# Kernel optimization log

Measured on AMD Instinct MI355X. Metric: run time of the kernel, lower is better.

The kernel has to match this reference:

```python
import jax, jax.numpy as jnp
import numpy as np

DIM = 384
HEADS = 6
NEG = -1e9  # masked-score fill; equivalent to gathering only kept K/V rows


def setup_inputs() -> dict:
    key = jax.random.key(0)
    ks = jax.random.split(key, 9)
    B, N, C = 1, 4098, DIM
    x = jax.random.normal(ks[0], (B, N, C), dtype=jnp.float32)
    pos = jax.random.normal(ks[1], (B, N + 1, C), dtype=jnp.float32)
    # float mask in [0,1); >=0.5 means 'foreground / keep as key', <0.5 pooled into back token
    mask = jax.random.uniform(ks[2], (B, 1, N - 2), dtype=jnp.float32)
    mask_block = jnp.ones((N + 1,), dtype=jnp.float32)  # positions 0, N-1, N always kept
    Wq = jax.random.normal(ks[3], (C, C), dtype=jnp.float32) * 0.02
    Wk = jax.random.normal(ks[4], (C, C), dtype=jnp.float32) * 0.02
    Wv = jax.random.normal(ks[5], (C, C), dtype=jnp.float32) * 0.02
    Wp = jax.random.normal(ks[6], (C, C), dtype=jnp.float32) * 0.02
    bp = jnp.zeros((C,), dtype=jnp.float32)
    return {"x": x, "pos": pos, "mask": mask, "mask_block": mask_block,
            "Wq": Wq, "Wk": Wk, "Wv": Wv, "Wp": Wp, "bp": bp}


def reference(x, pos, mask, mask_block, Wq, Wk, Wv, Wp, bp):
    B, N, C = x.shape
    H = HEADS
    D = C // H
    scale = D ** -0.5
    eps = 1e-10

    # back token: average of background (mask < 0.5) interior tokens
    reverse = jnp.where(mask < 0.5, 1.0, 0.0)                      # (B,1,N-2)
    pooled = jnp.einsum('bon,bnc->boc', reverse, x[:, 1:N - 1])    # (B,1,C)
    back_tokens = pooled / (reverse.sum(axis=2, keepdims=True) + eps)

    kv_x = jnp.concatenate([x, back_tokens], axis=1)               # (B,N+1,C)
    q_x = x + pos[:, :N]
    k_x = kv_x + pos

    q = (q_x @ Wq.T).reshape(B, N, H, D).transpose(0, 2, 1, 3)       # (B,H,N,D)
    k = (k_x @ Wk.T).reshape(B, N + 1, H, D).transpose(0, 2, 1, 3)   # (B,H,N+1,D)
    v = (kv_x @ Wv.T).reshape(B, N + 1, H, D).transpose(0, 2, 1, 3)  # (B,H,N+1,D)

    # key-selection mask: original gathers rows with mask_block >= 0.5;
    # masked softmax over all N+1 keys is mathematically identical.
    mb = mask_block.at[1:N - 1].set(mask[0, 0])
    keep = mb >= 0.5                                               # (N+1,)

    scores = jnp.einsum('bhqd,bhkd->bhqk', q, k) * scale
    scores = jnp.where(keep[None, None, None, :], scores, NEG)
    attn = jax.nn.softmax(scores, axis=-1)
    out = jnp.einsum('bhqk,bhkd->bhqd', attn, v)
    out = out.transpose(0, 2, 1, 3).reshape(B, N, C)
    return out @ Wp.T + bp
```

## Files before the change

### kernel.cpp

```cpp
#include <hip/hip_runtime.h>
#include <math.h>

#define N_TOK 4098
#define NK_TOK 4099
#define C_DIM 384
#define NKPAD 4160
#define NSLICE 5

typedef short  bh8 __attribute__((ext_vector_type(8)));
typedef float  f32x4 __attribute__((ext_vector_type(4)));
typedef unsigned short ushort;
typedef ushort u4 __attribute__((ext_vector_type(4)));
typedef ushort u8 __attribute__((ext_vector_type(8)));

static __device__ __forceinline__ ushort f2bf(float f) {
  unsigned int u = __float_as_uint(f);
  u = (u + 0x7FFF + ((u >> 16) & 1)) >> 16;
  return (ushort)u;
}
static __device__ __forceinline__ float bf2f(ushort s) {
  return __uint_as_float(((unsigned int)s) << 16);
}

#define QSCALE 0.18033688011112042f

__global__ __launch_bounds__(256) void prep_kernel(
    const float* __restrict__ x, const float* __restrict__ pos,
    const float* __restrict__ Wq, const float* __restrict__ Wk,
    const float* __restrict__ Wv, const float* __restrict__ Wp,
    const float* __restrict__ mask, const float* __restrict__ mask_block,
    ushort* __restrict__ Ak, ushort* __restrict__ Av,
    ushort* __restrict__ Wb, int* __restrict__ nk, int* __restrict__ inv,
    float* __restrict__ pooled_part, float* __restrict__ cnt_part) {
  const int b = blockIdx.x, t = threadIdx.x;
  if (b < 260) {
    const int r0 = b * 16;
#pragma unroll
    for (int i = 0; i < 6; ++i) {
      const int idx = i * 1024 + t * 4;
      const int row = r0 + idx / C_DIM, col = idx % C_DIM;
      if (row >= NK_TOK - 1) continue;
      const float4 pv = *(const float4*)&pos[(size_t)row * C_DIM + col];
      const float4 xv = *(const float4*)&x[(size_t)row * C_DIM + col];
      u4 k4 = {f2bf(xv.x + pv.x), f2bf(xv.y + pv.y),
               f2bf(xv.z + pv.z), f2bf(xv.w + pv.w)};
      *(u4*)&Ak[(size_t)row * C_DIM + col] = k4;
      u4 v4 = {f2bf(xv.x), f2bf(xv.y), f2bf(xv.z), f2bf(xv.w)};
      *(u4*)&Av[(size_t)row * C_DIM + col] = v4;
    }
  } else if (b < 292) {
    const int wi = b - 260;
    const float* src = (wi < 8) ? Wq : (wi < 16) ? Wk : (wi < 24) ? Wv : Wp;
    const float sc = (wi < 8) ? QSCALE : 1.f;
    const int base = (wi >> 3) * 147456 + (wi & 7) * 18432;
#pragma unroll 2
    for (int i = 0; i < 18; ++i) {
      const int g = base + i * 1024 + t * 4;
      const float4 v = *(const float4*)&src[(wi & 7) * 18432 + i * 1024 + t * 4];
      u4 o = {f2bf(v.x * sc), f2bf(v.y * sc), f2bf(v.z * sc), f2bf(v.w * sc)};
      *(u4*)&Wb[g] = o;
    }
  } else if (b == 292) {
    __shared__ int scnt[256];
    const int j0 = t * 17;
    unsigned int bits = 0;
    int c = 0;
#pragma unroll 1
    for (int u = 0; u < 17; ++u) {
      const int j = j0 + u;
      bool keep = false;
      if (j < NK_TOK)
        keep = (j >= 1 && j <= N_TOK - 2) ? (mask[j - 1] >= 0.5f)
                                          : (mask_block[j] >= 0.5f);
      if (keep) { bits |= 1u << u; ++c; }
    }
    scnt[t] = c;
    __syncthreads();
    for (int d = 1; d < 256; d <<= 1) {
      const int v = scnt[t];
      const int add = (t >= d) ? scnt[t - d] : 0;
      __syncthreads();
      scnt[t] = v + add;
      __syncthreads();
    }
    int base = scnt[t] - c;
    if (t == 255) *nk = scnt[255];
#pragma unroll 1
    for (int u = 0; u < 17; ++u) {
      const int j = j0 + u;
      if (j < NK_TOK) inv[j] = ((bits >> u) & 1) ? base++ : -1;
    }
  } else {
    const int pb = b - 293;
    const int r0 = pb * 64;
    float acc0 = 0.f, acc1 = 0.f;
    int lc = 0;
    for (int r = r0; r < r0 + 64; ++r) {
      if (mask[r] < 0.5f) {
        acc0 += x[(size_t)(r + 1) * C_DIM + t];
        if (t < 128) acc1 += x[(size_t)(r + 1) * C_DIM + 256 + t];
        ++lc;
      }
    }
    pooled_part[pb * C_DIM + t] = acc0;
    if (t < 128) pooled_part[pb * C_DIM + 256 + t] = acc1;
    if (t == 0) cnt_part[pb] = (float)lc;
  }
}

static __device__ __forceinline__ void gemm_core(
    const ushort* __restrict__ A, const ushort* __restrict__ B,
    ushort (* __restrict__ As)[72], ushort (* __restrict__ Bs)[72],
    int t, int w, int quad, int l15, f32x4 acc[4]) {
  const int g = t & 7;
  u8 ra[2], rb[2];
#pragma unroll
  for (int it = 0; it < 2; ++it) {
    const int r = it * 32 + (t >> 3);
    ra[it] = *(const u8*)&A[r * C_DIM + g * 8];
    rb[it] = *(const u8*)&B[r * C_DIM + g * 8];
  }
#pragma unroll 1
  for (int kt = 0; kt < 6; ++kt) {
    __syncthreads();
#pragma unroll
    for (int it = 0; it < 2; ++it) {
      const int r = it * 32 + (t >> 3);
      *(u8*)&As[r][g * 8] = ra[it];
      *(u8*)&Bs[r][g * 8] = rb[it];
    }
    __syncthreads();
    if (kt < 5) {
      const int k0 = (kt + 1) * 64;
#pragma unroll
      for (int it = 0; it < 2; ++it) {
        const int r = it * 32 + (t >> 3);
        ra[it] = *(const u8*)&A[r * C_DIM + k0 + g * 8];
        rb[it] = *(const u8*)&B[r * C_DIM + k0 + g * 8];
      }
    }
    const bh8 b0 = *(const bh8*)&Bs[w * 16 + l15][quad * 8];
    const bh8 b1 = *(const bh8*)&Bs[w * 16 + l15][32 + quad * 8];
#pragma unroll
    for (int mb = 0; mb < 4; ++mb) {
      const bh8 a0 = *(const bh8*)&As[mb * 16 + l15][quad * 8];
      const bh8 a1 = *(const bh8*)&As[mb * 16 + l15][32 + quad * 8];
      acc[mb] = __builtin_amdgcn_mfma_f32_16x16x32_bf16(a0, b0, acc[mb], 0, 0, 0);
      acc[mb] = __builtin_amdgcn_mfma_f32_16x16x32_bf16(a1, b1, acc[mb], 0, 0, 0);
    }
  }
}

__global__ __launch_bounds__(256) void gemm3_kernel(
    ushort* __restrict__ Ak, ushort* __restrict__ Av,
    const ushort* __restrict__ Wb, const int* __restrict__ inv,
    const float* __restrict__ pooled_part, const float* __restrict__ cnt_part,
    const float* __restrict__ pos,
    ushort* __restrict__ Qh, ushort* __restrict__ Kc, ushort* __restrict__ Vt) {
  __shared__ ushort As[64][72], Bs[64][72];
  const int t = threadIdx.x, w = t >> 6, lane = t & 63;
  const int quad = lane >> 4, l15 = lane & 15;
  const int m0 = blockIdx.x * 64;
  const int which = blockIdx.y / 6, h = blockIdx.y % 6;

  if (blockIdx.x == 64 && which >= 1) {
    float cs = 0.f;
#pragma unroll
    for (int p = 0; p < 64; ++p) cs += cnt_part[p];
    const float ic = 1.f / (cs + 1e-10f);
    for (int c = t; c < C_DIM; c += 256) {
      float s = 0.f;
      for (int p = 0; p < 64; ++p) s += pooled_part[p * C_DIM + c];
      const float back = s * ic;
      const size_t off = (size_t)(NK_TOK - 1) * C_DIM + c;
      if (which == 1) Ak[off] = f2bf(back + pos[off]);
      else            Av[off] = f2bf(back);
    }
    __syncthreads();
  }

  const ushort* A = (which == 2 ? Av : Ak) + (size_t)m0 * C_DIM;
  const ushort* B = Wb + (size_t)which * 147456 + (size_t)h * 64 * C_DIM;
  f32x4 acc[4];
#pragma unroll
  for (int i = 0; i < 4; ++i) acc[i] = (f32x4){0.f, 0.f, 0.f, 0.f};
  gemm_core(A, B, As, Bs, t, w, quad, l15, acc);
  const int n = w * 16 + l15;
  if (which == 0) {
#pragma unroll
    for (int mb = 0; mb < 4; ++mb)
#pragma unroll
      for (int r = 0; r < 4; ++r) {
        const int m = m0 + mb * 16 + quad * 4 + r;
        if (m < N_TOK) Qh[((size_t)h * N_TOK + m) * 64 + n] = f2bf(acc[mb][r]);
      }
  } else if (which == 1) {
#pragma unroll
    for (int mb = 0; mb < 4; ++mb)
#pragma unroll
      for (int r = 0; r < 4; ++r) {
        const int m = m0 + mb * 16 + quad * 4 + r;
        if (m < NK_TOK) {
          const int slot = inv[m];
          if (slot >= 0) Kc[((size_t)h * NKPAD + slot) * 64 + n] = f2bf(acc[mb][r]);
        }
      }
  } else {
#pragma unroll
    for (int mb = 0; mb < 4; ++mb)
#pragma unroll
      for (int r = 0; r < 4; ++r) {
        const int m = m0 + mb * 16 + quad * 4 + r;
        if (m < NK_TOK) {
          const int slot = inv[m];
          if (slot >= 0) Vt[((size_t)h * 64 + n) * NKPAD + slot] = f2bf(acc[mb][r]);
        }
      }
  }
}

__global__ __launch_bounds__(256) void gemm_out_kernel(
    const ushort* __restrict__ Am, const ushort* __restrict__ Wpb,
    const float* __restrict__ bp, float* __restrict__ out) {
  __shared__ ushort As[64][72], Bs[64][72];
  const int t = threadIdx.x, w = t >> 6, lane = t & 63;
  const int quad = lane >> 4, l15 = lane & 15;
  const int m0 = blockIdx.x * 64;
  const int h = blockIdx.y;
  f32x4 acc[4];
#pragma unroll
  for (int i = 0; i < 4; ++i) acc[i] = (f32x4){0.f, 0.f, 0.f, 0.f};
  gemm_core(Am + (size_t)m0 * C_DIM, Wpb + (size_t)h * 64 * C_DIM,
            As, Bs, t, w, quad, l15, acc);
  const int n = w * 16 + l15;
  const float bb = bp[h * 64 + n];
#pragma unroll
  for (int mb = 0; mb < 4; ++mb)
#pragma unroll
    for (int r = 0; r < 4; ++r) {
      const int m = m0 + mb * 16 + quad * 4 + r;
      if (m < N_TOK) out[(size_t)m * C_DIM + h * 64 + n] = acc[mb][r] + bb;
    }
}

__global__ __launch_bounds__(512) void attn_kernel(
    const ushort* __restrict__ Qh, const ushort* __restrict__ Kc,
    const ushort* __restrict__ Vt, const int* __restrict__ nkp,
    ushort* __restrict__ Opart, float* __restrict__ Lpart) {
  __shared__ ushort Ks[64][72];
  __shared__ ushort Vs[64][72];
  __shared__ ushort Ps[8][32][72];
  const int t = threadIdx.x, w = t >> 6, lane = t & 63;
  const int quad = lane >> 4, l15 = lane & 15;
  const int h = blockIdx.y, slice = blockIdx.z;
  const int q0 = blockIdx.x * 256;
  const int nk = *nkp, nchunk = (nk + 63) >> 6;
  const int g = t & 7;
  const int sr = t >> 3;

  bh8 qf[2][2];
#pragma unroll
  for (int qa = 0; qa < 2; ++qa) {
    int qr = q0 + w * 32 + qa * 16 + l15;
    if (qr > N_TOK - 1) qr = N_TOK - 1;
    const ushort* qp = Qh + ((size_t)h * N_TOK + qr) * 64 + quad * 8;
    qf[qa][0] = *(const bh8*)qp;
    qf[qa][1] = *(const bh8*)(qp + 32);
  }
  f32x4 oacc[2][4];
#pragma unroll
  for (int qa = 0; qa < 2; ++qa)
#pragma unroll
    for (int i = 0; i < 4; ++i) oacc[qa][i] = (f32x4){0.f, 0.f, 0.f, 0.f};
  float l_r[2] = {0.f, 0.f};

  const ushort* kb = Kc + (size_t)h * NKPAD * 64;
  const ushort* vb = Vt + (size_t)h * 64 * NKPAD;

  const ushort* kstage = kb + ((size_t)slice * 64 + sr) * 64 + g * 8;
  const ushort* vstage = vb + (size_t)sr * NKPAD + slice * 64 + g * 8;

  u8 rk, rv;
  if (slice < nchunk) {
    rk = *(const u8*)kstage;
    rv = *(const u8*)vstage;
  }
#pragma unroll 1
  for (int kc = slice; kc < nchunk; kc += NSLICE) {
    __syncthreads();
    *(u8*)&Ks[sr][g * 8] = rk;
    *(u8*)&Vs[sr][g * 8] = rv;
    __syncthreads();
    if (kc + NSLICE < nchunk) {
      kstage += NSLICE * 64 * 64;
      vstage += NSLICE * 64;
      rk = *(const u8*)kstage;
      rv = *(const u8*)vstage;
    }
    float csum[2] = {0.f, 0.f};
    if ((kc + 1) * 64 <= nk) {
#pragma unroll
      for (int f = 0; f < 4; ++f) {
        const bh8 a0 = *(const bh8*)&Ks[f * 16 + l15][quad * 8];
        const bh8 a1 = *(const bh8*)&Ks[f * 16 + l15][32 + quad * 8];
        f32x4 s4[2];
#pragma unroll
        for (int qa = 0; qa < 2; ++qa) {
          s4[qa] = (f32x4){0.f, 0.f, 0.f, 0.f};
          s4[qa] = __builtin_amdgcn_mfma_f32_16x16x32_bf16(a0, qf[qa][0], s4[qa], 0, 0, 0);
          s4[qa] = __builtin_amdgcn_mfma_f32_16x16x32_bf16(a1, qf[qa][1], s4[qa], 0, 0, 0);
        }
#pragma unroll
        for (int qa = 0; qa < 2; ++qa) {
          const float p0 = __builtin_amdgcn_exp2f(s4[qa][0]);
          const float p1 = __builtin_amdgcn_exp2f(s4[qa][1]);
          const float p2 = __builtin_amdgcn_exp2f(s4[qa][2]);
          const float p3 = __builtin_amdgcn_exp2f(s4[qa][3]);
          csum[qa] += (p0 + p1) + (p2 + p3);
          unsigned int lo, hi;
          asm("v_cvt_pk_bf16_f32 %0, %1, %2" : "=v"(lo) : "v"(p0), "v"(p1));
          asm("v_cvt_pk_bf16_f32 %0, %1, %2" : "=v"(hi) : "v"(p2), "v"(p3));
          uint2 pk;
          pk.x = lo; pk.y = hi;
          *(uint2*)&Ps[w][qa * 16 + l15][f * 16 + quad * 4] = pk;
        }
      }
    } else {
#pragma unroll
      for (int f = 0; f < 4; ++f) {
        const bh8 a0 = *(const bh8*)&Ks[f * 16 + l15][quad * 8];
        const bh8 a1 = *(const bh8*)&Ks[f * 16 + l15][32 + quad * 8];
        f32x4 s4[2];
#pragma unroll
        for (int qa = 0; qa < 2; ++qa) {
          s4[qa] = (f32x4){0.f, 0.f, 0.f, 0.f};
          s4[qa] = __builtin_amdgcn_mfma_f32_16x16x32_bf16(a0, qf[qa][0], s4[qa], 0, 0, 0);
          s4[qa] = __builtin_amdgcn_mfma_f32_16x16x32_bf16(a1, qf[qa][1], s4[qa], 0, 0, 0);
        }
        const int keyb = kc * 64 + f * 16 + quad * 4;
#pragma unroll
        for (int qa = 0; qa < 2; ++qa) {
          const float p0 = (keyb + 0 < nk) ? __builtin_amdgcn_exp2f(s4[qa][0]) : 0.f;
          const float p1 = (keyb + 1 < nk) ? __builtin_amdgcn_exp2f(s4[qa][1]) : 0.f;
          const float p2 = (keyb + 2 < nk) ? __builtin_amdgcn_exp2f(s4[qa][2]) : 0.f;
          const float p3 = (keyb + 3 < nk) ? __builtin_amdgcn_exp2f(s4[qa][3]) : 0.f;
          csum[qa] += (p0 + p1) + (p2 + p3);
          unsigned int lo, hi;
          asm("v_cvt_pk_bf16_f32 %0, %1, %2" : "=v"(lo) : "v"(p0), "v"(p1));
          asm("v_cvt_pk_bf16_f32 %0, %1, %2" : "=v"(hi) : "v"(p2), "v"(p3));
          uint2 pk;
          pk.x = lo; pk.y = hi;
          *(uint2*)&Ps[w][qa * 16 + l15][f * 16 + quad * 4] = pk;
        }
      }
    }
#pragma unroll
    for (int qa = 0; qa < 2; ++qa) {
      csum[qa] += __shfl_xor(csum[qa], 16);
      csum[qa] += __shfl_xor(csum[qa], 32);
      l_r[qa] += csum[qa];
    }

    bh8 pa[2][2];
#pragma unroll
    for (int qa = 0; qa < 2; ++qa) {
      pa[qa][0] = *(const bh8*)&Ps[w][qa * 16 + l15][quad * 8];
      pa[qa][1] = *(const bh8*)&Ps[w][qa * 16 + l15][32 + quad * 8];
    }
#pragma unroll
    for (int db = 0; db < 4; ++db) {
      const bh8 b0 = *(const bh8*)&Vs[db * 16 + l15][quad * 8];
      const bh8 b1 = *(const bh8*)&Vs[db * 16 + l15][32 + quad * 8];
#pragma unroll
      for (int qa = 0; qa < 2; ++qa) {
        oacc[qa][db] = __builtin_amdgcn_mfma_f32_16x16x32_bf16(pa[qa][0], b0, oacc[qa][db], 0, 0, 0);
        oacc[qa][db] = __builtin_amdgcn_mfma_f32_16x16x32_bf16(pa[qa][1], b1, oacc[qa][db], 0, 0, 0);
      }
    }
  }

  const int sh = slice * 6 + h;
#pragma unroll
  for (int qa = 0; qa < 2; ++qa) {
    const int qg = q0 + w * 32 + qa * 16;
#pragma unroll
    for (int db = 0; db < 4; ++db)
#pragma unroll
      for (int r = 0; r < 4; ++r) {
        const int q = qg + quad * 4 + r;
        if (q < N_TOK)
          Opart[((size_t)sh * NKPAD + q) * 64 + db * 16 + l15] = f2bf(oacc[qa][db][r]);
      }
    if (quad == 0) {
      const int q = qg + l15;
      if (q < N_TOK) Lpart[sh * NKPAD + q] = l_r[qa];
    }
  }
}

__global__ __launch_bounds__(256) void merge_kernel(const ushort* __restrict__ Opart,
                                                    const float* __restrict__ Lpart,
                                                    ushort* __restrict__ Am) {
  const int idx = blockIdx.x * 256 + threadIdx.x;
  if (idx >= N_TOK * 48) return;
  const int q = idx / 48, c = (idx % 48) * 8;
  const int h = c >> 6, d = c & 63;
  float l = 0.f;
#pragma unroll
  for (int s = 0; s < NSLICE; ++s) l += Lpart[(s * 6 + h) * NKPAD + q];
  const float inv = 1.f / l;
  float o[8] = {0.f, 0.f, 0.f, 0.f, 0.f, 0.f, 0.f, 0.f};
#pragma unroll
  for (int s = 0; s < NSLICE; ++s) {
    const u8 v = *(const u8*)&Opart[((size_t)(s * 6 + h) * NKPAD + q) * 64 + d];
#pragma unroll
    for (int j = 0; j < 8; ++j) o[j] += bf2f(v[j]);
  }
  u8 r;
#pragma unroll
  for (int j = 0; j < 8; ++j) r[j] = f2bf(o[j] * inv);
  *(u8*)&Am[(size_t)q * C_DIM + c] = r;
}

extern "C" void kernel_launch(void* const* d_in, const int* in_sizes, int n_in,
                              void* d_out, int out_size, void* d_ws, size_t ws_size,
                              hipStream_t stream) {
  const float* x          = (const float*)d_in[0];
  const float* pos        = (const float*)d_in[1];
  const float* mask       = (const float*)d_in[2];
  const float* mask_block = (const float*)d_in[3];
  const float* Wq         = (const float*)d_in[4];
  const float* Wk         = (const float*)d_in[5];
  const float* Wv         = (const float*)d_in[6];
  const float* Wp         = (const float*)d_in[7];
  const float* bp         = (const float*)d_in[8];
  float* out = (float*)d_out;
  char* wsb = (char*)d_ws;

  float*  pooled_part = (float*)wsb;
  float*  cnt_part    = (float*)(wsb + 98304);
  int*    nk          = (int*)(wsb + 98560);
  int*    inv         = (int*)(wsb + 99072);
  ushort* Ak          = (ushort*)(wsb + 115712);
  ushort* Av          = (ushort*)(wsb + 3310592);
  ushort* Wb          = (ushort*)(wsb + 6505472);
  ushort* Qh          = (ushort*)(wsb + 7685120);
  ushort* Kc          = (ushort*)(wsb + 10832384);
  ushort* Vt          = (ushort*)(wsb + 14027264);
  ushort* Am          = (ushort*)(wsb + 17222144);
  ushort* Op          = (ushort*)(wsb + 20417024);
  float*  Lp          = (float*)(wsb + 36391424);

  prep_kernel<<<dim3(357), dim3(256), 0, stream>>>(x, pos, Wq, Wk, Wv, Wp,
                                                   mask, mask_block, Ak, Av,
                                                   Wb, nk, inv,
                                                   pooled_part, cnt_part);
  gemm3_kernel<<<dim3(65, 18), 256, 0, stream>>>(Ak, Av, Wb, inv,
                                                 pooled_part, cnt_part, pos,
                                                 Qh, Kc, Vt);
  attn_kernel<<<dim3(17, 6, NSLICE), 512, 0, stream>>>(Qh, Kc, Vt, nk, Op, Lp);
  merge_kernel<<<dim3(769), 256, 0, stream>>>(Op, Lp, Am);
  gemm_out_kernel<<<dim3(65, 6), 256, 0, stream>>>(Am, Wb + 3 * 147456, bp, out);
}
```

Before: 142.8 us.

## Fuse split-K merge into attention via last-slice atomic counter

Removes the separate merge kernel. Each attention block bumps a per-(query tile, head) atomic counter, and the last of the slices to finish sums the partial outputs and row sums, then writes the normalized bf16 result to Am. The per-chunk cross-lane row-sum shuffles are also moved out of the key loop and done once at the end. This saves a kernel launch and a full pass over the partials in exchange for threadfences, atomics and a serialized tail merge on the last block.

```diff
diff --git a/kernel.cpp b/kernel.cpp
--- a/kernel.cpp
+++ b/kernel.cpp
@@ -31,7 +31,8 @@
     const float* __restrict__ mask, const float* __restrict__ mask_block,
     ushort* __restrict__ Ak, ushort* __restrict__ Av,
     ushort* __restrict__ Wb, int* __restrict__ nk, int* __restrict__ inv,
-    float* __restrict__ pooled_part, float* __restrict__ cnt_part) {
+    float* __restrict__ pooled_part, float* __restrict__ cnt_part,
+    int* __restrict__ mergeCnt) {
   const int b = blockIdx.x, t = threadIdx.x;
   if (b < 260) {
     const int r0 = b * 16;
@@ -61,6 +62,7 @@
       *(u4*)&Wb[g] = o;
     }
   } else if (b == 292) {
+    if (t < 102) mergeCnt[t] = 0;
     __shared__ int scnt[256];
     const int j0 = t * 17;
     unsigned int bits = 0;
@@ -246,7 +248,8 @@
 __global__ __launch_bounds__(512) void attn_kernel(
     const ushort* __restrict__ Qh, const ushort* __restrict__ Kc,
     const ushort* __restrict__ Vt, const int* __restrict__ nkp,
-    ushort* __restrict__ Opart, float* __restrict__ Lpart) {
+    ushort* __restrict__ Opart, float* __restrict__ Lpart,
+    int* __restrict__ mergeCnt, ushort* __restrict__ Am) {
   __shared__ ushort Ks[64][72];
   __shared__ ushort Vs[64][72];
   __shared__ ushort Ps[8][32][72];
@@ -297,7 +300,6 @@
       rk = *(const u8*)kstage;
       rv = *(const u8*)vstage;
     }
-    float csum[2] = {0.f, 0.f};
     if ((kc + 1) * 64 <= nk) {
 #pragma unroll
       for (int f = 0; f < 4; ++f) {
@@ -316,7 +318,7 @@
           const float p1 = __builtin_amdgcn_exp2f(s4[qa][1]);
           const float p2 = __builtin_amdgcn_exp2f(s4[qa][2]);
           const float p3 = __builtin_amdgcn_exp2f(s4[qa][3]);
-          csum[qa] += (p0 + p1) + (p2 + p3);
+          l_r[qa] += (p0 + p1) + (p2 + p3);
           unsigned int lo, hi;
           asm("v_cvt_pk_bf16_f32 %0, %1, %2" : "=v"(lo) : "v"(p0), "v"(p1));
           asm("v_cvt_pk_bf16_f32 %0, %1, %2" : "=v"(hi) : "v"(p2), "v"(p3));
@@ -344,7 +346,7 @@
           const float p1 = (keyb + 1 < nk) ? __builtin_amdgcn_exp2f(s4[qa][1]) : 0.f;
           const float p2 = (keyb + 2 < nk) ? __builtin_amdgcn_exp2f(s4[qa][2]) : 0.f;
           const float p3 = (keyb + 3 < nk) ? __builtin_amdgcn_exp2f(s4[qa][3]) : 0.f;
-          csum[qa] += (p0 + p1) + (p2 + p3);
+          l_r[qa] += (p0 + p1) + (p2 + p3);
           unsigned int lo, hi;
           asm("v_cvt_pk_bf16_f32 %0, %1, %2" : "=v"(lo) : "v"(p0), "v"(p1));
           asm("v_cvt_pk_bf16_f32 %0, %1, %2" : "=v"(hi) : "v"(p2), "v"(p3));
@@ -354,12 +356,6 @@
         }
       }
     }
-#pragma unroll
-    for (int qa = 0; qa < 2; ++qa) {
-      csum[qa] += __shfl_xor(csum[qa], 16);
-      csum[qa] += __shfl_xor(csum[qa], 32);
-      l_r[qa] += csum[qa];
-    }
 
     bh8 pa[2][2];
 #pragma unroll
@@ -382,6 +378,8 @@
   const int sh = slice * 6 + h;
 #pragma unroll
   for (int qa = 0; qa < 2; ++qa) {
+    l_r[qa] += __shfl_xor(l_r[qa], 16);
+    l_r[qa] += __shfl_xor(l_r[qa], 32);
     const int qg = q0 + w * 32 + qa * 16;
 #pragma unroll
     for (int db = 0; db < 4; ++db)
@@ -396,30 +394,36 @@
       if (q < N_TOK) Lpart[sh * NKPAD + q] = l_r[qa];
     }
   }
-}
-
-__global__ __launch_bounds__(256) void merge_kernel(const ushort* __restrict__ Opart,
-                                                    const float* __restrict__ Lpart,
-                                                    ushort* __restrict__ Am) {
-  const int idx = blockIdx.x * 256 + threadIdx.x;
-  if (idx >= N_TOK * 48) return;
-  const int q = idx / 48, c = (idx % 48) * 8;
-  const int h = c >> 6, d = c & 63;
-  float l = 0.f;
-#pragma unroll
-  for (int s = 0; s < NSLICE; ++s) l += Lpart[(s * 6 + h) * NKPAD + q];
-  const float inv = 1.f / l;
-  float o[8] = {0.f, 0.f, 0.f, 0.f, 0.f, 0.f, 0.f, 0.f};
-#pragma unroll
-  for (int s = 0; s < NSLICE; ++s) {
-    const u8 v = *(const u8*)&Opart[((size_t)(s * 6 + h) * NKPAD + q) * 64 + d];
-#pragma unroll
-    for (int j = 0; j < 8; ++j) o[j] += bf2f(v[j]);
-  }
-  u8 r;
-#pragma unroll
-  for (int j = 0; j < 8; ++j) r[j] = f2bf(o[j] * inv);
-  *(u8*)&Am[(size_t)q * C_DIM + c] = r;
+
+  __shared__ int is_last;
+  __threadfence();
+  __syncthreads();
+  if (t == 0) {
+    const int old = atomicAdd(&mergeCnt[blockIdx.x * 6 + h], 1);
+    is_last = ((old + 1) % NSLICE == 0);
+  }
+  __syncthreads();
+  if (!is_last) return;
+  __threadfence();
+  for (int idx = t; idx < 2048; idx += 512) {
+    const int q = q0 + (idx >> 3), d0 = (idx & 7) * 8;
+    if (q >= N_TOK) break;
+    float l = 0.f;
+#pragma unroll
+    for (int s = 0; s < NSLICE; ++s) l += Lpart[(s * 6 + h) * NKPAD + q];
+    const float invl = 1.f / l;
+    float o[8] = {0.f, 0.f, 0.f, 0.f, 0.f, 0.f, 0.f, 0.f};
+#pragma unroll
+    for (int s = 0; s < NSLICE; ++s) {
+      const u8 v = *(const u8*)&Opart[((size_t)(s * 6 + h) * NKPAD + q) * 64 + d0];
+#pragma unroll
+      for (int j = 0; j < 8; ++j) o[j] += bf2f(v[j]);
+    }
+    u8 r8;
+#pragma unroll
+    for (int j = 0; j < 8; ++j) r8[j] = f2bf(o[j] * invl);
+    *(u8*)&Am[(size_t)q * C_DIM + h * 64 + d0] = r8;
+  }
 }
 
 extern "C" void kernel_launch(void* const* d_in, const int* in_sizes, int n_in,
@@ -450,15 +454,17 @@
   ushort* Am          = (ushort*)(wsb + 17222144);
   ushort* Op          = (ushort*)(wsb + 20417024);
   float*  Lp          = (float*)(wsb + 36391424);
+  int*    mergeCnt    = (int*)(wsb + 36890624);
 
   prep_kernel<<<dim3(357), dim3(256), 0, stream>>>(x, pos, Wq, Wk, Wv, Wp,
                                                    mask, mask_block, Ak, Av,
                                                    Wb, nk, inv,
-                                                   pooled_part, cnt_part);
+                                                   pooled_part, cnt_part,
+                                                   mergeCnt);
   gemm3_kernel<<<dim3(65, 18), 256, 0, stream>>>(Ak, Av, Wb, inv,
                                                  pooled_part, cnt_part, pos,
                                                  Qh, Kc, Vt);
-  attn_kernel<<<dim3(17, 6, NSLICE), 512, 0, stream>>>(Qh, Kc, Vt, nk, Op, Lp);
-  merge_kernel<<<dim3(769), 256, 0, stream>>>(Op, Lp, Am);
+  attn_kernel<<<dim3(17, 6, NSLICE), 512, 0, stream>>>(Qh, Kc, Vt, nk, Op, Lp,
+                                                       mergeCnt, Am);
   gemm_out_kernel<<<dim3(65, 6), 256, 0, stream>>>(Am, Wb + 3 * 147456, bp, out);
 }
```

New measurement: 293.5 us. 106% more time.
